# Kernel optimization log

Measured on AMD Instinct MI355X. Metric: run time of the kernel, lower is better.

The kernel has to match this reference:

```python
import jax, jax.numpy as jnp
import numpy as np

IN_DIM, OUT_DIM = 96, 32
D = IN_DIM + OUT_DIM  # 128, feature dim of x
H, KQ = 8, 64         # head_num, KQ_dim
GAMMA = 1e-4


def setup_inputs() -> dict:
    key = jax.random.key(0)
    kx, kk, kq, kv = jax.random.split(key, 4)
    B, N = 32, 2048
    std_kq = (GAMMA / D) ** 0.5
    return {
        "x": jax.random.normal(kx, (B, N, D), dtype=jnp.float32),
        # nn.Linear weight shape [out_features, in_features]; stacked per head
        "Wk": jax.random.normal(kk, (H, KQ, D), dtype=jnp.float32) * std_kq,
        "Wq": jax.random.normal(kq, (H, KQ, D), dtype=jnp.float32) * std_kq,
        "Wv": jax.random.normal(kv, (H, D, D), dtype=jnp.float32) * GAMMA,
    }


def reference(x, Wk, Wq, Wv):
    # Per-head projections (nn.Linear: y = x @ W^T), stacked over heads h
    K = jnp.einsum("bnd,hkd->bhnk", x, Wk)  # [B,H,N,KQ]
    Q = jnp.einsum("bnd,hkd->bhnk", x, Wq)  # [B,H,N,KQ]
    V = jnp.einsum("bnd,hed->bhne", x, Wv)  # [B,H,N,D]
    # No softmax -> (Q K^T) V == Q (K^T V); use the O(n d^2) associative form
    KtV = jnp.einsum("bhnk,bhne->bhke", K, V)  # [B,H,KQ,D]
    # sum over heads folded into the contraction
    out = jnp.einsum("bhnk,bhke->bne", Q, KtV)  # [B,N,D]
    return out
```

## Files before the change

### kernel.cpp

```cpp
#include <hip/hip_runtime.h>

#define BB 32
#define NN 2048
#define DD 128
#define HH 8
#define KK 64

typedef __attribute__((ext_vector_type(8))) short bf16x8;
typedef __attribute__((ext_vector_type(4))) float f32x4;
#define MFMA_BF16 __builtin_amdgcn_mfma_f32_16x16x32_bf16


__device__ __forceinline__ float bf2f(unsigned short h){ return __uint_as_float(((unsigned)h) << 16); }
__device__ __forceinline__ unsigned short f2bf(float f){
  unsigned u = __float_as_uint(f);
  u += 0x7fffu + ((u >> 16) & 1u);
  return (unsigned short)(u >> 16);
}
__device__ __forceinline__ unsigned pack2(float a, float b){
  return (unsigned)f2bf(a) | ((unsigned)f2bf(b) << 16);
}

__device__ __forceinline__ bf16x8 ldfrag_sw(const unsigned short* base, int row16, int kc, int lane){
  int d = row16 + (lane & 15);
  int q = lane >> 4;
  int ch = ((kc << 2) + q) ^ (d & 7);
  return *(const bf16x8*)(base + d*128 + ch*8);
}

__global__ __launch_bounds__(512, 4) void kgkp(const float* __restrict__ x,
                                               const float* __restrict__ Wq,
                                               const float* __restrict__ Wk,
                                               unsigned short* __restrict__ Gp_bf,
                                               unsigned short* __restrict__ Pbf,
                                               unsigned short* __restrict__ x_bf){
  __shared__ __align__(16) unsigned short sm[32768];
  const int t = threadIdx.x;
  const int bid = blockIdx.x;
  const int w = t >> 6, lane = t & 63, quad = lane >> 4;
  if (bid < 256){
    unsigned short* xh = sm;
    unsigned short* xl = sm + 16384;
    const int b = bid & 31, chunk = bid >> 5;
    const int wr = (w >> 1)*32, wc = (w & 1)*64;
    f32x4 acc[2][4] = {};
    for (int sub = 0; sub < 2; ++sub){
      if (sub) __syncthreads();
      const float* xb = x + ((size_t)b*NN + (size_t)(chunk*256 + sub*128))*DD;
      unsigned short* xbo = x_bf + (((size_t)(b*16 + chunk*2 + sub)) << 14);
      for (int it = 0; it < 2; ++it){
        int gidx = it*512 + t;
        int n4g = (gidx & 7) | (((gidx >> 6) & 3) << 3);
        int dcq = ((gidx >> 3) & 7) | (((gidx >> 8) & 3) << 3);
        float4 v[4];
        #pragma unroll
        for (int j = 0; j < 4; ++j)
          v[j] = *(const float4*)(xb + (size_t)(n4g*4 + j)*DD + dcq*4);
        unsigned short hh[4][4], ll[4][4];
        #pragma unroll
        for (int j = 0; j < 4; ++j)
          #pragma unroll
          for (int i = 0; i < 4; ++i){
            float f = (&v[j].x)[i];
            unsigned short h = f2bf(f);
            hh[j][i] = h;
            ll[j][i] = f2bf(f - bf2f(h));
          }
        #pragma unroll
        for (int i = 0; i < 4; ++i){
          int d = dcq*4 + i;
          int off = d*128 + ((((n4g >> 1) ^ (d & 7)) << 3) + (n4g & 1)*4);
          *(ushort4*)(xh + off) = make_ushort4(hh[0][i], hh[1][i], hh[2][i], hh[3][i]);
          *(ushort4*)(xl + off) = make_ushort4(ll[0][i], ll[1][i], ll[2][i], ll[3][i]);
        }
        #pragma unroll
        for (int j = 0; j < 4; ++j){
          int n = n4g*4 + j;
          int off = n*128 + ((((dcq >> 1) ^ (n & 7)) << 3) + (dcq & 1)*4);
          *(ushort4*)(xbo + off) = make_ushort4(hh[j][0], hh[j][1], hh[j][2], hh[j][3]);
        }
      }
      __syncthreads();
      for (int kc = 0; kc < 4; ++kc){
        bf16x8 ah[2], al[2], bh[4], bl[4];
        #pragma unroll
        for (int r = 0; r < 2; ++r){
          ah[r] = ldfrag_sw(xh, wr + r*16, kc, lane);
          al[r] = ldfrag_sw(xl, wr + r*16, kc, lane);
        }
        #pragma unroll
        for (int c = 0; c < 4; ++c){
          bh[c] = ldfrag_sw(xh, wc + c*16, kc, lane);
          bl[c] = ldfrag_sw(xl, wc + c*16, kc, lane);
        }
        #pragma unroll
        for (int r = 0; r < 2; ++r)
          #pragma unroll
          for (int c = 0; c < 4; ++c){
            acc[r][c] = MFMA_BF16(ah[r], bh[c], acc[r][c], 0, 0, 0);
            acc[r][c] = MFMA_BF16(ah[r], bl[c], acc[r][c], 0, 0, 0);
            acc[r][c] = MFMA_BF16(al[r], bh[c], acc[r][c], 0, 0, 0);
          }
      }
    }
    __syncthreads();
    float* Sf = (float*)sm;
    #pragma unroll
    for (int r = 0; r < 2; ++r)
      #pragma unroll
      for (int c = 0; c < 4; ++c)
        #pragma unroll
        for (int reg = 0; reg < 4; ++reg)
          Sf[(wr + r*16 + quad*4 + reg)*128 + wc + c*16 + (lane & 15)] = acc[r][c][reg];
    __syncthreads();
    unsigned short* gp = Gp_bf + ((size_t)(chunk*32 + b) << 14);
    for (int i = t; i < 2048; i += 512){
      int r = i >> 4, c8 = (i & 15) * 8;
      const float* s = Sf + r*128 + c8;
      uint4 o;
      o.x = pack2(s[0], s[1]); o.y = pack2(s[2], s[3]);
      o.z = pack2(s[4], s[5]); o.w = pack2(s[6], s[7]);
      *(uint4*)(gp + r*128 + c8) = o;
    }
  } else {
    float* Aq = (float*)sm;
    float* Bk = Aq + 64*36;
    const int kpid = bid - 256;
    const int h = kpid >> 2, rt = kpid & 3;
    const int i0 = rt * 32;
    const int tr = t >> 6, tc = t & 63;
    const float* wq = Wq + h*KK*DD;
    const float* wk = Wk + h*KK*DD;
    for (int i = t; i < 512; i += 512){
      int k = i >> 3, c4 = (i & 7) << 2;
      *(float4*)(&Aq[k*36 + c4]) = *(const float4*)(wq + k*DD + i0 + c4);
    }
    for (int i = t; i < 2048; i += 512){
      int k = i >> 5, c4 = (i & 31) << 2;
      *(float4*)(&Bk[k*132 + c4]) = *(const float4*)(wk + k*DD + c4);
    }
    __syncthreads();
    float acc[4][2] = {};
    for (int k = 0; k < 64; k += 2){
      float a0[4], a1[4], b0[2], b1[2];
      *(float4*)a0 = *(float4*)(&Aq[k*36 + tr*4]);
      *(float4*)a1 = *(float4*)(&Aq[(k+1)*36 + tr*4]);
      b0[0] = Bk[k*132 + tc*2];     b0[1] = Bk[k*132 + tc*2 + 1];
      b1[0] = Bk[(k+1)*132 + tc*2]; b1[1] = Bk[(k+1)*132 + tc*2 + 1];
      #pragma unroll
      for (int i = 0; i < 4; ++i)
        #pragma unroll
        for (int j = 0; j < 2; ++j){
          acc[i][j] += a0[i]*b0[j];
          acc[i][j] += a1[i]*b1[j];
        }
    }
    unsigned short* Ph = Pbf + h*DD*DD;
    #pragma unroll
    for (int i = 0; i < 4; ++i){
      int r = i0 + tr*4 + i, c = tc*2;
      int off = r*128 + ((((c >> 3) ^ (r & 7)) << 3) + (c & 7));
      *(ushort2*)(&Ph[off]) = make_ushort2(f2bf(acc[i][0]), f2bf(acc[i][1]));
    }
  }
}

__global__ __launch_bounds__(256) void kgr(const unsigned short* __restrict__ Gp_bf,
                                           const float* __restrict__ Wv,
                                           unsigned short* __restrict__ G_bf,
                                           unsigned short* __restrict__ Wv_bf){
  const int bid = blockIdx.x, t = threadIdx.x;
  if (bid < 256){
    const int b = bid >> 3, strip = bid & 7;
    const int r = strip*16 + (t >> 4), ch = t & 15;
    float s[8] = {};
    #pragma unroll
    for (int p = 0; p < 8; ++p){
      uint4 u = *(const uint4*)(Gp_bf + (((size_t)(p*32 + b)) << 14) + r*128 + ch*8);
      const unsigned short* pu = (const unsigned short*)&u;
      #pragma unroll
      for (int j = 0; j < 8; ++j) s[j] += bf2f(pu[j]);
    }
    uint4 o;
    o.x = pack2(s[0], s[1]); o.y = pack2(s[2], s[3]);
    o.z = pack2(s[4], s[5]); o.w = pack2(s[6], s[7]);
    *(uint4*)(G_bf + ((size_t)b << 14) + r*128 + ((ch ^ (r & 7)) << 3)) = o;
  } else {
    const int h = bid - 256;
    const float* Wvh = Wv + (size_t)h*DD*DD;
    unsigned short* outp = Wv_bf + (size_t)h*DD*DD;
    for (int i = t; i < 4096; i += 256){
      int e = i >> 5, dc = (i & 31) * 4;
      float4 v = *(const float4*)(Wvh + (size_t)e*DD + dc);
      int off = e*128 + ((((dc >> 3) ^ (e & 7)) << 3) + (dc & 4));
      *(ushort4*)(outp + off) = make_ushort4(f2bf(v.x), f2bf(v.y), f2bf(v.z), f2bf(v.w));
    }
  }
}

__global__ __launch_bounds__(512, 2) void km2(const unsigned short* __restrict__ G_bf,
                                              const unsigned short* __restrict__ Wv_bf,
                                              const unsigned short* __restrict__ Pbf,
                                              unsigned short* __restrict__ Mp_bf){
  __shared__ __align__(16) unsigned short sm[32768];
  unsigned short* As = sm;
  unsigned short* Bs = sm + 16384;
  const int bid = blockIdx.x;
  const int b = bid & 31, h = bid >> 5;
  const int t = threadIdx.x;
  const int w = t >> 6, lane = t & 63, quad = lane >> 4;
  const unsigned short* Gb = G_bf + ((size_t)b << 14);
  const unsigned short* Wvh = Wv_bf + ((size_t)h << 14);
  for (int i = t; i < 2048; i += 512){
    *(uint4*)(As + i*8) = *(const uint4*)(Gb + i*8);
    *(uint4*)(Bs + i*8) = *(const uint4*)(Wvh + i*8);
  }
  __syncthreads();
  f32x4 acc1[8] = {};
  for (int kc = 0; kc < 4; ++kc){
    bf16x8 a = ldfrag_sw(As, w*16, kc, lane);
    bf16x8 bb[8];
    #pragma unroll
    for (int c = 0; c < 8; ++c) bb[c] = ldfrag_sw(Bs, c*16, kc, lane);
    #pragma unroll
    for (int c = 0; c < 8; ++c) acc1[c] = MFMA_BF16(a, bb[c], acc1[c], 0, 0, 0);
  }
  __syncthreads();
  #pragma unroll
  for (int c = 0; c < 8; ++c){
    int e = c*16 + (lane & 15);
    int d0 = w*16 + quad*4;
    int off = e*128 + ((((d0 >> 3) ^ (e & 7)) << 3) + (d0 & 7));
    *(ushort4*)(Bs + off) = make_ushort4(f2bf(acc1[c][0]), f2bf(acc1[c][1]),
                                         f2bf(acc1[c][2]), f2bf(acc1[c][3]));
  }
  const unsigned short* Ph = Pbf + (size_t)h*DD*DD;
  for (int i = t; i < 2048; i += 512)
    *(uint4*)(As + i*8) = *(const uint4*)(Ph + i*8);
  __syncthreads();
  f32x4 acc2[8] = {};
  for (int kc = 0; kc < 4; ++kc){
    bf16x8 a = ldfrag_sw(As, w*16, kc, lane);
    bf16x8 bb[8];
    #pragma unroll
    for (int c = 0; c < 8; ++c) bb[c] = ldfrag_sw(Bs, c*16, kc, lane);
    #pragma unroll
    for (int c = 0; c < 8; ++c) acc2[c] = MFMA_BF16(a, bb[c], acc2[c], 0, 0, 0);
  }
  __syncthreads();
  float* Sf = (float*)sm;
  #pragma unroll
  for (int c = 0; c < 8; ++c)
    #pragma unroll
    for (int reg = 0; reg < 4; ++reg)
      Sf[(w*16 + quad*4 + reg)*128 + c*16 + (lane & 15)] = acc2[c][reg];
  __syncthreads();
  unsigned short* Mb = Mp_bf + (((size_t)(b*8 + h)) << 14);
  for (int i = t; i < 2048; i += 512){
    int r = i >> 4, c8 = (i & 15) * 8;
    const float* s = Sf + r*128 + c8;
    uint4 o;
    o.x = pack2(s[0], s[1]); o.y = pack2(s[2], s[3]);
    o.z = pack2(s[4], s[5]); o.w = pack2(s[6], s[7]);
    *(uint4*)(Mb + r*128 + c8) = o;
  }
}

__global__ __launch_bounds__(256) void kmr(const unsigned short* __restrict__ Mp_bf,
                                           unsigned short* __restrict__ Mt_sw){
  __shared__ float Sf[16][132];
  const int bid = blockIdx.x;
  const int b = bid >> 3, es = bid & 7;
  const int t = threadIdx.x;
  {
    int d = t >> 1, half = t & 1;
    float s[8] = {};
    #pragma unroll
    for (int h = 0; h < 8; ++h){
      uint4 u = *(const uint4*)(Mp_bf + (((size_t)(b*8 + h)) << 14) + d*128 + es*16 + half*8);
      const unsigned short* pu = (const unsigned short*)&u;
      #pragma unroll
      for (int j = 0; j < 8; ++j) s[j] += bf2f(pu[j]);
    }
    #pragma unroll
    for (int j = 0; j < 8; ++j) Sf[half*8 + j][d] = s[j];
  }
  __syncthreads();
  unsigned short* Mb = Mt_sw + ((size_t)b << 14);
  {
    int el = t >> 4, ng = t & 15;
    int e = es*16 + el;
    const float* s = &Sf[el][ng*8];
    uint4 o;
    o.x = pack2(s[0], s[1]); o.y = pack2(s[2], s[3]);
    o.z = pack2(s[4], s[5]); o.w = pack2(s[6], s[7]);
    *(uint4*)(Mb + e*128 + ((ng ^ (e & 7)) << 3)) = o;
  }
}

__global__ __launch_bounds__(512, 4) void ko2(const unsigned short* __restrict__ x_bf,
                                              const unsigned short* __restrict__ Mt_sw,
                                              float* __restrict__ out){
  __shared__ __align__(16) unsigned short sm[32768];
  unsigned short* xs = sm;
  unsigned short* Ms = sm + 16384;
  const int bid = blockIdx.x;
  const int b = bid & 31, nt = bid >> 5;
  const int t = threadIdx.x;
  const int w = t >> 6, lane = t & 63, quad = lane >> 4;
  const unsigned short* xbf = x_bf + (((size_t)(b*16 + nt)) << 14);
  const unsigned short* Mtb = Mt_sw + ((size_t)b << 14);
  for (int i = t; i < 2048; i += 512){
    *(uint4*)(xs + i*8) = *(const uint4*)(xbf + i*8);
    *(uint4*)(Ms + i*8) = *(const uint4*)(Mtb + i*8);
  }
  __syncthreads();
  const int wr = (w >> 1)*32, wc = (w & 1)*64;
  f32x4 acc[2][4] = {};
  for (int kc = 0; kc < 4; ++kc){
    bf16x8 a[2], bb[4];
    #pragma unroll
    for (int r = 0; r < 2; ++r) a[r] = ldfrag_sw(xs, wr + r*16, kc, lane);
    #pragma unroll
    for (int c = 0; c < 4; ++c) bb[c] = ldfrag_sw(Ms, wc + c*16, kc, lane);
    #pragma unroll
    for (int r = 0; r < 2; ++r)
      #pragma unroll
      for (int c = 0; c < 4; ++c)
        acc[r][c] = MFMA_BF16(a[r], bb[c], acc[r][c], 0, 0, 0);
  }
  __syncthreads();
  float* Sf = (float*)sm;
  #pragma unroll
  for (int r = 0; r < 2; ++r)
    #pragma unroll
    for (int c = 0; c < 4; ++c)
      #pragma unroll
      for (int reg = 0; reg < 4; ++reg)
        Sf[(wr + r*16 + quad*4 + reg)*128 + wc + c*16 + (lane & 15)] = acc[r][c][reg];
  __syncthreads();
  float* ob = out + ((size_t)b*NN + (size_t)nt*128)*DD;
  for (int i = t; i < 4096; i += 512){
    int n = i >> 5, c4 = (i & 31) * 4;
    *(float4*)(ob + (size_t)n*DD + c4) = *(const float4*)(Sf + n*128 + c4);
  }
}

extern "C" void kernel_launch(void* const* d_in, const int* in_sizes, int n_in,
                              void* d_out, int out_size, void* d_ws, size_t ws_size,
                              hipStream_t stream){
  const float* x  = (const float*)d_in[0];
  const float* Wk = (const float*)d_in[1];
  const float* Wq = (const float*)d_in[2];
  const float* Wv = (const float*)d_in[3];
  float* out = (float*)d_out;
  unsigned short* wsu = (unsigned short*)d_ws;
  unsigned short* Gp_bf = wsu;
  unsigned short* G_bf  = wsu + 4194304;
  unsigned short* Pbf   = wsu + 4718592;
  unsigned short* Wv_bf = wsu + 4849664;
  unsigned short* Mp_bf = wsu + 4980736;
  unsigned short* Mt_sw = wsu + 9175040;
  unsigned short* x_bf  = wsu + 9699328;

  kgkp<<<288, 512, 0, stream>>>(x, Wq, Wk, Gp_bf, Pbf, x_bf);
  kgr <<<264, 256, 0, stream>>>(Gp_bf, Wv, G_bf, Wv_bf);
  km2 <<<256, 512, 0, stream>>>(G_bf, Wv_bf, Pbf, Mp_bf);
  kmr <<<256, 256, 0, stream>>>(Mp_bf, Mt_sw);
  ko2 <<<512, 512, 0, stream>>>(x_bf, Mt_sw, out);
}
```

Baseline: 126.2 us.

## Fuse five kernel launches into one cooperative kernel with grid syncs

Merges the five pipeline kernels (Gram partials, reduction, M computation, head reduction, output GEMM) into a single cooperative kernel of 256 blocks separated by grid.sync barriers. The G reduction and the Wv bf16 conversion now happen directly into shared memory inside the M stage, which drops the G_bf/Wv_bf global round trips. The P computation is folded into the first 32 blocks, and the output stage processes two tiles per block. This removes launch gaps and some global traffic, but the final GEMM now has fewer resident blocks, grid barriers add cost, and the first 32 blocks carry extra serial work.

```diff
diff --git a/kernel.cpp b/kernel.cpp
--- a/kernel.cpp
+++ b/kernel.cpp
@@ -1,9 +1,10 @@
 #include <hip/hip_runtime.h>
-
-#define BB 32
+#include <hip/hip_cooperative_groups.h>
+
+namespace cg = cooperative_groups;
+
 #define NN 2048
 #define DD 128
-#define HH 8
 #define KK 64
 
 typedef __attribute__((ext_vector_type(8))) short bf16x8;
@@ -28,17 +29,21 @@
   return *(const bf16x8*)(base + d*128 + ch*8);
 }
 
-__global__ __launch_bounds__(512, 4) void kgkp(const float* __restrict__ x,
-                                               const float* __restrict__ Wq,
-                                               const float* __restrict__ Wk,
-                                               unsigned short* __restrict__ Gp_bf,
-                                               unsigned short* __restrict__ Pbf,
-                                               unsigned short* __restrict__ x_bf){
+__global__ __launch_bounds__(512, 2) void fused_all(
+    const float* __restrict__ x,  const float* __restrict__ Wq,
+    const float* __restrict__ Wk, const float* __restrict__ Wv,
+    float* __restrict__ out,
+    unsigned short* __restrict__ Gp_bf, unsigned short* __restrict__ Pbf,
+    unsigned short* __restrict__ Mp_bf, unsigned short* __restrict__ Mt_sw,
+    unsigned short* __restrict__ x_bf)
+{
   __shared__ __align__(16) unsigned short sm[32768];
   const int t = threadIdx.x;
   const int bid = blockIdx.x;
   const int w = t >> 6, lane = t & 63, quad = lane >> 4;
-  if (bid < 256){
+  cg::grid_group grid = cg::this_grid();
+
+  {
     unsigned short* xh = sm;
     unsigned short* xl = sm + 16384;
     const int b = bid & 31, chunk = bid >> 5;
@@ -122,227 +127,204 @@
       o.z = pack2(s[4], s[5]); o.w = pack2(s[6], s[7]);
       *(uint4*)(gp + r*128 + c8) = o;
     }
-  } else {
-    float* Aq = (float*)sm;
-    float* Bk = Aq + 64*36;
-    const int kpid = bid - 256;
-    const int h = kpid >> 2, rt = kpid & 3;
-    const int i0 = rt * 32;
-    const int tr = t >> 6, tc = t & 63;
-    const float* wq = Wq + h*KK*DD;
-    const float* wk = Wk + h*KK*DD;
-    for (int i = t; i < 512; i += 512){
-      int k = i >> 3, c4 = (i & 7) << 2;
-      *(float4*)(&Aq[k*36 + c4]) = *(const float4*)(wq + k*DD + i0 + c4);
-    }
+    if (bid < 32){
+      __syncthreads();
+      float* Aq = (float*)sm;
+      float* Bk = Aq + 64*36;
+      const int h = bid >> 2, rt = bid & 3;
+      const int i0 = rt * 32;
+      const int tr = t >> 6, tc = t & 63;
+      const float* wq = Wq + h*KK*DD;
+      const float* wk = Wk + h*KK*DD;
+      for (int i = t; i < 512; i += 512){
+        int k = i >> 3, c4 = (i & 7) << 2;
+        *(float4*)(&Aq[k*36 + c4]) = *(const float4*)(wq + k*DD + i0 + c4);
+      }
+      for (int i = t; i < 2048; i += 512){
+        int k = i >> 5, c4 = (i & 31) << 2;
+        *(float4*)(&Bk[k*132 + c4]) = *(const float4*)(wk + k*DD + c4);
+      }
+      __syncthreads();
+      float acc2[4][2] = {};
+      for (int k = 0; k < 64; k += 2){
+        float a0[4], a1[4], b0[2], b1[2];
+        *(float4*)a0 = *(float4*)(&Aq[k*36 + tr*4]);
+        *(float4*)a1 = *(float4*)(&Aq[(k+1)*36 + tr*4]);
+        b0[0] = Bk[k*132 + tc*2];     b0[1] = Bk[k*132 + tc*2 + 1];
+        b1[0] = Bk[(k+1)*132 + tc*2]; b1[1] = Bk[(k+1)*132 + tc*2 + 1];
+        #pragma unroll
+        for (int i = 0; i < 4; ++i)
+          #pragma unroll
+          for (int j = 0; j < 2; ++j){
+            acc2[i][j] += a0[i]*b0[j];
+            acc2[i][j] += a1[i]*b1[j];
+          }
+      }
+      unsigned short* Ph = Pbf + h*DD*DD;
+      #pragma unroll
+      for (int i = 0; i < 4; ++i){
+        int r = i0 + tr*4 + i, c = tc*2;
+        int off = r*128 + ((((c >> 3) ^ (r & 7)) << 3) + (c & 7));
+        *(ushort2*)(&Ph[off]) = make_ushort2(f2bf(acc2[i][0]), f2bf(acc2[i][1]));
+      }
+    }
+  }
+  __threadfence();
+  grid.sync();
+
+  {
+    unsigned short* As = sm;
+    unsigned short* Bs = sm + 16384;
+    const int b = bid & 31, h = bid >> 5;
     for (int i = t; i < 2048; i += 512){
-      int k = i >> 5, c4 = (i & 31) << 2;
-      *(float4*)(&Bk[k*132 + c4]) = *(const float4*)(wk + k*DD + c4);
-    }
-    __syncthreads();
-    float acc[4][2] = {};
-    for (int k = 0; k < 64; k += 2){
-      float a0[4], a1[4], b0[2], b1[2];
-      *(float4*)a0 = *(float4*)(&Aq[k*36 + tr*4]);
-      *(float4*)a1 = *(float4*)(&Aq[(k+1)*36 + tr*4]);
-      b0[0] = Bk[k*132 + tc*2];     b0[1] = Bk[k*132 + tc*2 + 1];
-      b1[0] = Bk[(k+1)*132 + tc*2]; b1[1] = Bk[(k+1)*132 + tc*2 + 1];
-      #pragma unroll
-      for (int i = 0; i < 4; ++i)
-        #pragma unroll
-        for (int j = 0; j < 2; ++j){
-          acc[i][j] += a0[i]*b0[j];
-          acc[i][j] += a1[i]*b1[j];
-        }
-    }
-    unsigned short* Ph = Pbf + h*DD*DD;
-    #pragma unroll
-    for (int i = 0; i < 4; ++i){
-      int r = i0 + tr*4 + i, c = tc*2;
-      int off = r*128 + ((((c >> 3) ^ (r & 7)) << 3) + (c & 7));
-      *(ushort2*)(&Ph[off]) = make_ushort2(f2bf(acc[i][0]), f2bf(acc[i][1]));
-    }
-  }
-}
-
-__global__ __launch_bounds__(256) void kgr(const unsigned short* __restrict__ Gp_bf,
-                                           const float* __restrict__ Wv,
-                                           unsigned short* __restrict__ G_bf,
-                                           unsigned short* __restrict__ Wv_bf){
-  const int bid = blockIdx.x, t = threadIdx.x;
-  if (bid < 256){
-    const int b = bid >> 3, strip = bid & 7;
-    const int r = strip*16 + (t >> 4), ch = t & 15;
-    float s[8] = {};
-    #pragma unroll
-    for (int p = 0; p < 8; ++p){
-      uint4 u = *(const uint4*)(Gp_bf + (((size_t)(p*32 + b)) << 14) + r*128 + ch*8);
-      const unsigned short* pu = (const unsigned short*)&u;
-      #pragma unroll
-      for (int j = 0; j < 8; ++j) s[j] += bf2f(pu[j]);
-    }
-    uint4 o;
-    o.x = pack2(s[0], s[1]); o.y = pack2(s[2], s[3]);
-    o.z = pack2(s[4], s[5]); o.w = pack2(s[6], s[7]);
-    *(uint4*)(G_bf + ((size_t)b << 14) + r*128 + ((ch ^ (r & 7)) << 3)) = o;
-  } else {
-    const int h = bid - 256;
+      int r = i >> 4, c8 = (i & 15) * 8;
+      float s[8] = {};
+      #pragma unroll
+      for (int p = 0; p < 8; ++p){
+        uint4 u = *(const uint4*)(Gp_bf + (((size_t)(p*32 + b)) << 14) + r*128 + c8);
+        const unsigned short* pu = (const unsigned short*)&u;
+        #pragma unroll
+        for (int j = 0; j < 8; ++j) s[j] += bf2f(pu[j]);
+      }
+      uint4 o;
+      o.x = pack2(s[0], s[1]); o.y = pack2(s[2], s[3]);
+      o.z = pack2(s[4], s[5]); o.w = pack2(s[6], s[7]);
+      *(uint4*)(As + r*128 + ((((c8 >> 3) ^ (r & 7))) << 3)) = o;
+    }
     const float* Wvh = Wv + (size_t)h*DD*DD;
-    unsigned short* outp = Wv_bf + (size_t)h*DD*DD;
-    for (int i = t; i < 4096; i += 256){
+    for (int i = t; i < 4096; i += 512){
       int e = i >> 5, dc = (i & 31) * 4;
       float4 v = *(const float4*)(Wvh + (size_t)e*DD + dc);
       int off = e*128 + ((((dc >> 3) ^ (e & 7)) << 3) + (dc & 4));
-      *(ushort4*)(outp + off) = make_ushort4(f2bf(v.x), f2bf(v.y), f2bf(v.z), f2bf(v.w));
+      *(ushort4*)(Bs + off) = make_ushort4(f2bf(v.x), f2bf(v.y), f2bf(v.z), f2bf(v.w));
+    }
+    __syncthreads();
+    f32x4 acc1[8] = {};
+    for (int kc = 0; kc < 4; ++kc){
+      bf16x8 a = ldfrag_sw(As, w*16, kc, lane);
+      bf16x8 bb[8];
+      #pragma unroll
+      for (int c = 0; c < 8; ++c) bb[c] = ldfrag_sw(Bs, c*16, kc, lane);
+      #pragma unroll
+      for (int c = 0; c < 8; ++c) acc1[c] = MFMA_BF16(a, bb[c], acc1[c], 0, 0, 0);
+    }
+    __syncthreads();
+    #pragma unroll
+    for (int c = 0; c < 8; ++c){
+      int e = c*16 + (lane & 15);
+      int d0 = w*16 + quad*4;
+      int off = e*128 + ((((d0 >> 3) ^ (e & 7)) << 3) + (d0 & 7));
+      *(ushort4*)(Bs + off) = make_ushort4(f2bf(acc1[c][0]), f2bf(acc1[c][1]),
+                                           f2bf(acc1[c][2]), f2bf(acc1[c][3]));
+    }
+    const unsigned short* Ph = Pbf + (size_t)h*DD*DD;
+    for (int i = t; i < 2048; i += 512)
+      *(uint4*)(As + i*8) = *(const uint4*)(Ph + i*8);
+    __syncthreads();
+    f32x4 acc2[8] = {};
+    for (int kc = 0; kc < 4; ++kc){
+      bf16x8 a = ldfrag_sw(As, w*16, kc, lane);
+      bf16x8 bb[8];
+      #pragma unroll
+      for (int c = 0; c < 8; ++c) bb[c] = ldfrag_sw(Bs, c*16, kc, lane);
+      #pragma unroll
+      for (int c = 0; c < 8; ++c) acc2[c] = MFMA_BF16(a, bb[c], acc2[c], 0, 0, 0);
+    }
+    __syncthreads();
+    float* Sf = (float*)sm;
+    #pragma unroll
+    for (int c = 0; c < 8; ++c)
+      #pragma unroll
+      for (int reg = 0; reg < 4; ++reg)
+        Sf[(w*16 + quad*4 + reg)*128 + c*16 + (lane & 15)] = acc2[c][reg];
+    __syncthreads();
+    unsigned short* Mb = Mp_bf + (((size_t)(b*8 + h)) << 14);
+    for (int i = t; i < 2048; i += 512){
+      int r = i >> 4, c8 = (i & 15) * 8;
+      const float* s = Sf + r*128 + c8;
+      uint4 o;
+      o.x = pack2(s[0], s[1]); o.y = pack2(s[2], s[3]);
+      o.z = pack2(s[4], s[5]); o.w = pack2(s[6], s[7]);
+      *(uint4*)(Mb + r*128 + c8) = o;
     }
   }
-}
-
-__global__ __launch_bounds__(512, 2) void km2(const unsigned short* __restrict__ G_bf,
-                                              const unsigned short* __restrict__ Wv_bf,
-                                              const unsigned short* __restrict__ Pbf,
-                                              unsigned short* __restrict__ Mp_bf){
-  __shared__ __align__(16) unsigned short sm[32768];
-  unsigned short* As = sm;
-  unsigned short* Bs = sm + 16384;
-  const int bid = blockIdx.x;
-  const int b = bid & 31, h = bid >> 5;
-  const int t = threadIdx.x;
-  const int w = t >> 6, lane = t & 63, quad = lane >> 4;
-  const unsigned short* Gb = G_bf + ((size_t)b << 14);
-  const unsigned short* Wvh = Wv_bf + ((size_t)h << 14);
-  for (int i = t; i < 2048; i += 512){
-    *(uint4*)(As + i*8) = *(const uint4*)(Gb + i*8);
-    *(uint4*)(Bs + i*8) = *(const uint4*)(Wvh + i*8);
+  __threadfence();
+  grid.sync();
+
+  {
+    const int rb = bid >> 3, es = bid & 7;
+    float* Rf = (float*)sm;
+    {
+      int d = t >> 2, q = t & 3;
+      float s[4] = {};
+      #pragma unroll
+      for (int h = 0; h < 8; ++h){
+        uint2 u = *(const uint2*)(Mp_bf + (((size_t)(rb*8 + h)) << 14) + d*128 + es*16 + q*4);
+        const unsigned short* pu = (const unsigned short*)&u;
+        #pragma unroll
+        for (int j = 0; j < 4; ++j) s[j] += bf2f(pu[j]);
+      }
+      #pragma unroll
+      for (int j = 0; j < 4; ++j) Rf[(q*4 + j)*132 + d] = s[j];
+    }
+    __syncthreads();
+    unsigned short* Mb = Mt_sw + ((size_t)rb << 14);
+    if (t < 256){
+      int el = t >> 4, ng = t & 15;
+      int e = es*16 + el;
+      const float* s2 = &Rf[el*132 + ng*8];
+      uint4 o;
+      o.x = pack2(s2[0], s2[1]); o.y = pack2(s2[2], s2[3]);
+      o.z = pack2(s2[4], s2[5]); o.w = pack2(s2[6], s2[7]);
+      *(uint4*)(Mb + e*128 + ((ng ^ (e & 7)) << 3)) = o;
+    }
   }
-  __syncthreads();
-  f32x4 acc1[8] = {};
-  for (int kc = 0; kc < 4; ++kc){
-    bf16x8 a = ldfrag_sw(As, w*16, kc, lane);
-    bf16x8 bb[8];
-    #pragma unroll
-    for (int c = 0; c < 8; ++c) bb[c] = ldfrag_sw(Bs, c*16, kc, lane);
-    #pragma unroll
-    for (int c = 0; c < 8; ++c) acc1[c] = MFMA_BF16(a, bb[c], acc1[c], 0, 0, 0);
-  }
-  __syncthreads();
-  #pragma unroll
-  for (int c = 0; c < 8; ++c){
-    int e = c*16 + (lane & 15);
-    int d0 = w*16 + quad*4;
-    int off = e*128 + ((((d0 >> 3) ^ (e & 7)) << 3) + (d0 & 7));
-    *(ushort4*)(Bs + off) = make_ushort4(f2bf(acc1[c][0]), f2bf(acc1[c][1]),
-                                         f2bf(acc1[c][2]), f2bf(acc1[c][3]));
-  }
-  const unsigned short* Ph = Pbf + (size_t)h*DD*DD;
-  for (int i = t; i < 2048; i += 512)
-    *(uint4*)(As + i*8) = *(const uint4*)(Ph + i*8);
-  __syncthreads();
-  f32x4 acc2[8] = {};
-  for (int kc = 0; kc < 4; ++kc){
-    bf16x8 a = ldfrag_sw(As, w*16, kc, lane);
-    bf16x8 bb[8];
-    #pragma unroll
-    for (int c = 0; c < 8; ++c) bb[c] = ldfrag_sw(Bs, c*16, kc, lane);
-    #pragma unroll
-    for (int c = 0; c < 8; ++c) acc2[c] = MFMA_BF16(a, bb[c], acc2[c], 0, 0, 0);
-  }
-  __syncthreads();
-  float* Sf = (float*)sm;
-  #pragma unroll
-  for (int c = 0; c < 8; ++c)
-    #pragma unroll
-    for (int reg = 0; reg < 4; ++reg)
-      Sf[(w*16 + quad*4 + reg)*128 + c*16 + (lane & 15)] = acc2[c][reg];
-  __syncthreads();
-  unsigned short* Mb = Mp_bf + (((size_t)(b*8 + h)) << 14);
-  for (int i = t; i < 2048; i += 512){
-    int r = i >> 4, c8 = (i & 15) * 8;
-    const float* s = Sf + r*128 + c8;
-    uint4 o;
-    o.x = pack2(s[0], s[1]); o.y = pack2(s[2], s[3]);
-    o.z = pack2(s[4], s[5]); o.w = pack2(s[6], s[7]);
-    *(uint4*)(Mb + r*128 + c8) = o;
-  }
-}
-
-__global__ __launch_bounds__(256) void kmr(const unsigned short* __restrict__ Mp_bf,
-                                           unsigned short* __restrict__ Mt_sw){
-  __shared__ float Sf[16][132];
-  const int bid = blockIdx.x;
-  const int b = bid >> 3, es = bid & 7;
-  const int t = threadIdx.x;
+  __threadfence();
+  grid.sync();
+
   {
-    int d = t >> 1, half = t & 1;
-    float s[8] = {};
-    #pragma unroll
-    for (int h = 0; h < 8; ++h){
-      uint4 u = *(const uint4*)(Mp_bf + (((size_t)(b*8 + h)) << 14) + d*128 + es*16 + half*8);
-      const unsigned short* pu = (const unsigned short*)&u;
-      #pragma unroll
-      for (int j = 0; j < 8; ++j) s[j] += bf2f(pu[j]);
-    }
-    #pragma unroll
-    for (int j = 0; j < 8; ++j) Sf[half*8 + j][d] = s[j];
-  }
-  __syncthreads();
-  unsigned short* Mb = Mt_sw + ((size_t)b << 14);
-  {
-    int el = t >> 4, ng = t & 15;
-    int e = es*16 + el;
-    const float* s = &Sf[el][ng*8];
-    uint4 o;
-    o.x = pack2(s[0], s[1]); o.y = pack2(s[2], s[3]);
-    o.z = pack2(s[4], s[5]); o.w = pack2(s[6], s[7]);
-    *(uint4*)(Mb + e*128 + ((ng ^ (e & 7)) << 3)) = o;
-  }
-}
-
-__global__ __launch_bounds__(512, 4) void ko2(const unsigned short* __restrict__ x_bf,
-                                              const unsigned short* __restrict__ Mt_sw,
-                                              float* __restrict__ out){
-  __shared__ __align__(16) unsigned short sm[32768];
-  unsigned short* xs = sm;
-  unsigned short* Ms = sm + 16384;
-  const int bid = blockIdx.x;
-  const int b = bid & 31, nt = bid >> 5;
-  const int t = threadIdx.x;
-  const int w = t >> 6, lane = t & 63, quad = lane >> 4;
-  const unsigned short* xbf = x_bf + (((size_t)(b*16 + nt)) << 14);
-  const unsigned short* Mtb = Mt_sw + ((size_t)b << 14);
-  for (int i = t; i < 2048; i += 512){
-    *(uint4*)(xs + i*8) = *(const uint4*)(xbf + i*8);
-    *(uint4*)(Ms + i*8) = *(const uint4*)(Mtb + i*8);
-  }
-  __syncthreads();
-  const int wr = (w >> 1)*32, wc = (w & 1)*64;
-  f32x4 acc[2][4] = {};
-  for (int kc = 0; kc < 4; ++kc){
-    bf16x8 a[2], bb[4];
-    #pragma unroll
-    for (int r = 0; r < 2; ++r) a[r] = ldfrag_sw(xs, wr + r*16, kc, lane);
-    #pragma unroll
-    for (int c = 0; c < 4; ++c) bb[c] = ldfrag_sw(Ms, wc + c*16, kc, lane);
-    #pragma unroll
-    for (int r = 0; r < 2; ++r)
-      #pragma unroll
-      for (int c = 0; c < 4; ++c)
-        acc[r][c] = MFMA_BF16(a[r], bb[c], acc[r][c], 0, 0, 0);
-  }
-  __syncthreads();
-  float* Sf = (float*)sm;
-  #pragma unroll
-  for (int r = 0; r < 2; ++r)
-    #pragma unroll
-    for (int c = 0; c < 4; ++c)
-      #pragma unroll
-      for (int reg = 0; reg < 4; ++reg)
-        Sf[(wr + r*16 + quad*4 + reg)*128 + wc + c*16 + (lane & 15)] = acc[r][c][reg];
-  __syncthreads();
-  float* ob = out + ((size_t)b*NN + (size_t)nt*128)*DD;
-  for (int i = t; i < 4096; i += 512){
-    int n = i >> 5, c4 = (i & 31) * 4;
-    *(float4*)(ob + (size_t)n*DD + c4) = *(const float4*)(Sf + n*128 + c4);
+    const int b = bid & 31, ntb = (bid >> 5) * 2;
+    const unsigned short* Mtb = Mt_sw + ((size_t)b << 14);
+    for (int nt = ntb; nt < ntb + 2; ++nt){
+      __syncthreads();
+      unsigned short* xs = sm;
+      unsigned short* Ms = sm + 16384;
+      const unsigned short* xbf = x_bf + (((size_t)(b*16 + nt)) << 14);
+      for (int i = t; i < 2048; i += 512){
+        *(uint4*)(xs + i*8) = *(const uint4*)(xbf + i*8);
+        *(uint4*)(Ms + i*8) = *(const uint4*)(Mtb + i*8);
+      }
+      __syncthreads();
+      const int wr = (w >> 1)*32, wc = (w & 1)*64;
+      f32x4 acc[2][4] = {};
+      for (int kc = 0; kc < 4; ++kc){
+        bf16x8 a[2], bb[4];
+        #pragma unroll
+        for (int r = 0; r < 2; ++r) a[r] = ldfrag_sw(xs, wr + r*16, kc, lane);
+        #pragma unroll
+        for (int c = 0; c < 4; ++c) bb[c] = ldfrag_sw(Ms, wc + c*16, kc, lane);
+        #pragma unroll
+        for (int r = 0; r < 2; ++r)
+          #pragma unroll
+          for (int c = 0; c < 4; ++c)
+            acc[r][c] = MFMA_BF16(a[r], bb[c], acc[r][c], 0, 0, 0);
+      }
+      __syncthreads();
+      float* Sf = (float*)sm;
+      #pragma unroll
+      for (int r = 0; r < 2; ++r)
+        #pragma unroll
+        for (int c = 0; c < 4; ++c)
+          #pragma unroll
+          for (int reg = 0; reg < 4; ++reg)
+            Sf[(wr + r*16 + quad*4 + reg)*128 + wc + c*16 + (lane & 15)] = acc[r][c][reg];
+      __syncthreads();
+      float* ob = out + ((size_t)b*NN + (size_t)nt*128)*DD;
+      for (int i = t; i < 4096; i += 512){
+        int n = i >> 5, c4 = (i & 31) * 4;
+        *(float4*)(ob + (size_t)n*DD + c4) = *(const float4*)(Sf + n*128 + c4);
+      }
+    }
   }
 }
 
@@ -356,16 +338,12 @@
   float* out = (float*)d_out;
   unsigned short* wsu = (unsigned short*)d_ws;
   unsigned short* Gp_bf = wsu;
-  unsigned short* G_bf  = wsu + 4194304;
-  unsigned short* Pbf   = wsu + 4718592;
-  unsigned short* Wv_bf = wsu + 4849664;
-  unsigned short* Mp_bf = wsu + 4980736;
-  unsigned short* Mt_sw = wsu + 9175040;
-  unsigned short* x_bf  = wsu + 9699328;
-
-  kgkp<<<288, 512, 0, stream>>>(x, Wq, Wk, Gp_bf, Pbf, x_bf);
-  kgr <<<264, 256, 0, stream>>>(Gp_bf, Wv, G_bf, Wv_bf);
-  km2 <<<256, 512, 0, stream>>>(G_bf, Wv_bf, Pbf, Mp_bf);
-  kmr <<<256, 256, 0, stream>>>(Mp_bf, Mt_sw);
-  ko2 <<<512, 512, 0, stream>>>(x_bf, Mt_sw, out);
-}
+  unsigned short* Pbf   = wsu + 4194304;
+  unsigned short* Mp_bf = wsu + 4325376;
+  unsigned short* Mt_sw = wsu + 8519680;
+  unsigned short* x_bf  = wsu + 9043968;
+
+  void* args[] = { (void*)&x, (void*)&Wq, (void*)&Wk, (void*)&Wv, (void*)&out,
+                   (void*)&Gp_bf, (void*)&Pbf, (void*)&Mp_bf, (void*)&Mt_sw, (void*)&x_bf };
+  hipLaunchCooperativeKernel((const void*)fused_all, dim3(256), dim3(512), args, 0, stream);
+}
```

Result: slower. 359.9 us (+185.2%).

## Fuse Gram reduction and Wv conversion into km2, split Gram over more blocks

Applied to the files above, without the earlier changes.

The Gram-matrix kernel now launches 512 blocks of 128 rows each instead of 256 blocks of 256 rows, which gives more parallelism. The separate reduce/convert kernel is removed: km2 now sums the 16 partial Gram matrices and converts its Wv slice to bf16 straight into shared memory. km2 is also split over two output-column halves to reach 512 blocks with higher occupancy. The cost is redundant work: each km2 block re-reads all 16 partials, so the reduction traffic is duplicated across heads and halves, and Wv is converted repeatedly.

```diff
diff --git a/kernel.cpp b/kernel.cpp
--- a/kernel.cpp
+++ b/kernel.cpp
@@ -1,9 +1,7 @@
 #include <hip/hip_runtime.h>
 
-#define BB 32
 #define NN 2048
 #define DD 128
-#define HH 8
 #define KK 64
 
 typedef __attribute__((ext_vector_type(8))) short bf16x8;
@@ -38,70 +36,67 @@
   const int t = threadIdx.x;
   const int bid = blockIdx.x;
   const int w = t >> 6, lane = t & 63, quad = lane >> 4;
-  if (bid < 256){
+  if (bid < 512){
     unsigned short* xh = sm;
     unsigned short* xl = sm + 16384;
     const int b = bid & 31, chunk = bid >> 5;
     const int wr = (w >> 1)*32, wc = (w & 1)*64;
     f32x4 acc[2][4] = {};
-    for (int sub = 0; sub < 2; ++sub){
-      if (sub) __syncthreads();
-      const float* xb = x + ((size_t)b*NN + (size_t)(chunk*256 + sub*128))*DD;
-      unsigned short* xbo = x_bf + (((size_t)(b*16 + chunk*2 + sub)) << 14);
-      for (int it = 0; it < 2; ++it){
-        int gidx = it*512 + t;
-        int n4g = (gidx & 7) | (((gidx >> 6) & 3) << 3);
-        int dcq = ((gidx >> 3) & 7) | (((gidx >> 8) & 3) << 3);
-        float4 v[4];
-        #pragma unroll
-        for (int j = 0; j < 4; ++j)
-          v[j] = *(const float4*)(xb + (size_t)(n4g*4 + j)*DD + dcq*4);
-        unsigned short hh[4][4], ll[4][4];
-        #pragma unroll
-        for (int j = 0; j < 4; ++j)
-          #pragma unroll
-          for (int i = 0; i < 4; ++i){
-            float f = (&v[j].x)[i];
-            unsigned short h = f2bf(f);
-            hh[j][i] = h;
-            ll[j][i] = f2bf(f - bf2f(h));
-          }
+    const float* xb = x + ((size_t)b*NN + (size_t)chunk*128)*DD;
+    unsigned short* xbo = x_bf + (((size_t)(b*16 + chunk)) << 14);
+    for (int it = 0; it < 2; ++it){
+      int gidx = it*512 + t;
+      int n4g = (gidx & 7) | (((gidx >> 6) & 3) << 3);
+      int dcq = ((gidx >> 3) & 7) | (((gidx >> 8) & 3) << 3);
+      float4 v[4];
+      #pragma unroll
+      for (int j = 0; j < 4; ++j)
+        v[j] = *(const float4*)(xb + (size_t)(n4g*4 + j)*DD + dcq*4);
+      unsigned short hh[4][4], ll[4][4];
+      #pragma unroll
+      for (int j = 0; j < 4; ++j)
         #pragma unroll
         for (int i = 0; i < 4; ++i){
-          int d = dcq*4 + i;
-          int off = d*128 + ((((n4g >> 1) ^ (d & 7)) << 3) + (n4g & 1)*4);
-          *(ushort4*)(xh + off) = make_ushort4(hh[0][i], hh[1][i], hh[2][i], hh[3][i]);
-          *(ushort4*)(xl + off) = make_ushort4(ll[0][i], ll[1][i], ll[2][i], ll[3][i]);
+          float f = (&v[j].x)[i];
+          unsigned short h = f2bf(f);
+          hh[j][i] = h;
+          ll[j][i] = f2bf(f - bf2f(h));
         }
-        #pragma unroll
-        for (int j = 0; j < 4; ++j){
-          int n = n4g*4 + j;
-          int off = n*128 + ((((dcq >> 1) ^ (n & 7)) << 3) + (dcq & 1)*4);
-          *(ushort4*)(xbo + off) = make_ushort4(hh[j][0], hh[j][1], hh[j][2], hh[j][3]);
-        }
+      #pragma unroll
+      for (int i = 0; i < 4; ++i){
+        int d = dcq*4 + i;
+        int off = d*128 + ((((n4g >> 1) ^ (d & 7)) << 3) + (n4g & 1)*4);
+        *(ushort4*)(xh + off) = make_ushort4(hh[0][i], hh[1][i], hh[2][i], hh[3][i]);
+        *(ushort4*)(xl + off) = make_ushort4(ll[0][i], ll[1][i], ll[2][i], ll[3][i]);
       }
-      __syncthreads();
-      for (int kc = 0; kc < 4; ++kc){
-        bf16x8 ah[2], al[2], bh[4], bl[4];
-        #pragma unroll
-        for (int r = 0; r < 2; ++r){
-          ah[r] = ldfrag_sw(xh, wr + r*16, kc, lane);
-          al[r] = ldfrag_sw(xl, wr + r*16, kc, lane);
-        }
+      #pragma unroll
+      for (int j = 0; j < 4; ++j){
+        int n = n4g*4 + j;
+        int off = n*128 + ((((dcq >> 1) ^ (n & 7)) << 3) + (dcq & 1)*4);
+        *(ushort4*)(xbo + off) = make_ushort4(hh[j][0], hh[j][1], hh[j][2], hh[j][3]);
+      }
+    }
+    __syncthreads();
+    for (int kc = 0; kc < 4; ++kc){
+      bf16x8 ah[2], al[2], bh[4], bl[4];
+      #pragma unroll
+      for (int r = 0; r < 2; ++r){
+        ah[r] = ldfrag_sw(xh, wr + r*16, kc, lane);
+        al[r] = ldfrag_sw(xl, wr + r*16, kc, lane);
+      }
+      #pragma unroll
+      for (int c = 0; c < 4; ++c){
+        bh[c] = ldfrag_sw(xh, wc + c*16, kc, lane);
+        bl[c] = ldfrag_sw(xl, wc + c*16, kc, lane);
+      }
+      #pragma unroll
+      for (int r = 0; r < 2; ++r)
         #pragma unroll
         for (int c = 0; c < 4; ++c){
-          bh[c] = ldfrag_sw(xh, wc + c*16, kc, lane);
-          bl[c] = ldfrag_sw(xl, wc + c*16, kc, lane);
+          acc[r][c] = MFMA_BF16(ah[r], bh[c], acc[r][c], 0, 0, 0);
+          acc[r][c] = MFMA_BF16(ah[r], bl[c], acc[r][c], 0, 0, 0);
+          acc[r][c] = MFMA_BF16(al[r], bh[c], acc[r][c], 0, 0, 0);
         }
-        #pragma unroll
-        for (int r = 0; r < 2; ++r)
-          #pragma unroll
-          for (int c = 0; c < 4; ++c){
-            acc[r][c] = MFMA_BF16(ah[r], bh[c], acc[r][c], 0, 0, 0);
-            acc[r][c] = MFMA_BF16(ah[r], bl[c], acc[r][c], 0, 0, 0);
-            acc[r][c] = MFMA_BF16(al[r], bh[c], acc[r][c], 0, 0, 0);
-          }
-      }
     }
     __syncthreads();
     float* Sf = (float*)sm;
@@ -125,7 +120,7 @@
   } else {
     float* Aq = (float*)sm;
     float* Bk = Aq + 64*36;
-    const int kpid = bid - 256;
+    const int kpid = bid - 512;
     const int h = kpid >> 2, rt = kpid & 3;
     const int i0 = rt * 32;
     const int tr = t >> 6, tc = t & 63;
@@ -165,18 +160,23 @@
   }
 }
 
-__global__ __launch_bounds__(256) void kgr(const unsigned short* __restrict__ Gp_bf,
-                                           const float* __restrict__ Wv,
-                                           unsigned short* __restrict__ G_bf,
-                                           unsigned short* __restrict__ Wv_bf){
-  const int bid = blockIdx.x, t = threadIdx.x;
-  if (bid < 256){
-    const int b = bid >> 3, strip = bid & 7;
-    const int r = strip*16 + (t >> 4), ch = t & 15;
+__global__ __launch_bounds__(512, 4) void km2(const unsigned short* __restrict__ Gp_bf,
+                                              const float* __restrict__ Wv,
+                                              const unsigned short* __restrict__ Pbf,
+                                              unsigned short* __restrict__ Mp_bf){
+  __shared__ __align__(16) unsigned short sm[24576];
+  unsigned short* As = sm;
+  unsigned short* Bs = sm + 16384;
+  const int bid = blockIdx.x;
+  const int b = bid & 31, h = (bid >> 5) & 7, eh = bid >> 8;
+  const int t = threadIdx.x;
+  const int w = t >> 6, lane = t & 63, quad = lane >> 4;
+  for (int i = t; i < 2048; i += 512){
+    int r = i >> 4, c8 = (i & 15) * 8;
     float s[8] = {};
     #pragma unroll
-    for (int p = 0; p < 8; ++p){
-      uint4 u = *(const uint4*)(Gp_bf + (((size_t)(p*32 + b)) << 14) + r*128 + ch*8);
+    for (int p = 0; p < 16; ++p){
+      uint4 u = *(const uint4*)(Gp_bf + (((size_t)(p*32 + b)) << 14) + r*128 + c8);
       const unsigned short* pu = (const unsigned short*)&u;
       #pragma unroll
       for (int j = 0; j < 8; ++j) s[j] += bf2f(pu[j]);
@@ -184,50 +184,28 @@
     uint4 o;
     o.x = pack2(s[0], s[1]); o.y = pack2(s[2], s[3]);
     o.z = pack2(s[4], s[5]); o.w = pack2(s[6], s[7]);
-    *(uint4*)(G_bf + ((size_t)b << 14) + r*128 + ((ch ^ (r & 7)) << 3)) = o;
-  } else {
-    const int h = bid - 256;
-    const float* Wvh = Wv + (size_t)h*DD*DD;
-    unsigned short* outp = Wv_bf + (size_t)h*DD*DD;
-    for (int i = t; i < 4096; i += 256){
-      int e = i >> 5, dc = (i & 31) * 4;
-      float4 v = *(const float4*)(Wvh + (size_t)e*DD + dc);
-      int off = e*128 + ((((dc >> 3) ^ (e & 7)) << 3) + (dc & 4));
-      *(ushort4*)(outp + off) = make_ushort4(f2bf(v.x), f2bf(v.y), f2bf(v.z), f2bf(v.w));
-    }
-  }
-}
-
-__global__ __launch_bounds__(512, 2) void km2(const unsigned short* __restrict__ G_bf,
-                                              const unsigned short* __restrict__ Wv_bf,
-                                              const unsigned short* __restrict__ Pbf,
-                                              unsigned short* __restrict__ Mp_bf){
-  __shared__ __align__(16) unsigned short sm[32768];
-  unsigned short* As = sm;
-  unsigned short* Bs = sm + 16384;
-  const int bid = blockIdx.x;
-  const int b = bid & 31, h = bid >> 5;
-  const int t = threadIdx.x;
-  const int w = t >> 6, lane = t & 63, quad = lane >> 4;
-  const unsigned short* Gb = G_bf + ((size_t)b << 14);
-  const unsigned short* Wvh = Wv_bf + ((size_t)h << 14);
+    *(uint4*)(As + r*128 + ((((c8 >> 3) ^ (r & 7))) << 3)) = o;
+  }
+  const float* Wvh = Wv + (size_t)h*DD*DD + (size_t)eh*64*DD;
   for (int i = t; i < 2048; i += 512){
-    *(uint4*)(As + i*8) = *(const uint4*)(Gb + i*8);
-    *(uint4*)(Bs + i*8) = *(const uint4*)(Wvh + i*8);
-  }
-  __syncthreads();
-  f32x4 acc1[8] = {};
+    int el = i >> 5, dc = (i & 31) * 4;
+    float4 v = *(const float4*)(Wvh + (size_t)el*DD + dc);
+    int off = el*128 + ((((dc >> 3) ^ (el & 7)) << 3) + (dc & 4));
+    *(ushort4*)(Bs + off) = make_ushort4(f2bf(v.x), f2bf(v.y), f2bf(v.z), f2bf(v.w));
+  }
+  __syncthreads();
+  f32x4 acc1[4] = {};
   for (int kc = 0; kc < 4; ++kc){
     bf16x8 a = ldfrag_sw(As, w*16, kc, lane);
-    bf16x8 bb[8];
-    #pragma unroll
-    for (int c = 0; c < 8; ++c) bb[c] = ldfrag_sw(Bs, c*16, kc, lane);
-    #pragma unroll
-    for (int c = 0; c < 8; ++c) acc1[c] = MFMA_BF16(a, bb[c], acc1[c], 0, 0, 0);
+    bf16x8 bb[4];
+    #pragma unroll
+    for (int c = 0; c < 4; ++c) bb[c] = ldfrag_sw(Bs, c*16, kc, lane);
+    #pragma unroll
+    for (int c = 0; c < 4; ++c) acc1[c] = MFMA_BF16(a, bb[c], acc1[c], 0, 0, 0);
   }
   __syncthreads();
   #pragma unroll
-  for (int c = 0; c < 8; ++c){
+  for (int c = 0; c < 4; ++c){
     int e = c*16 + (lane & 15);
     int d0 = w*16 + quad*4;
     int off = e*128 + ((((d0 >> 3) ^ (e & 7)) << 3) + (d0 & 7));
@@ -238,27 +216,27 @@
   for (int i = t; i < 2048; i += 512)
     *(uint4*)(As + i*8) = *(const uint4*)(Ph + i*8);
   __syncthreads();
-  f32x4 acc2[8] = {};
+  f32x4 acc2[4] = {};
   for (int kc = 0; kc < 4; ++kc){
     bf16x8 a = ldfrag_sw(As, w*16, kc, lane);
-    bf16x8 bb[8];
-    #pragma unroll
-    for (int c = 0; c < 8; ++c) bb[c] = ldfrag_sw(Bs, c*16, kc, lane);
-    #pragma unroll
-    for (int c = 0; c < 8; ++c) acc2[c] = MFMA_BF16(a, bb[c], acc2[c], 0, 0, 0);
+    bf16x8 bb[4];
+    #pragma unroll
+    for (int c = 0; c < 4; ++c) bb[c] = ldfrag_sw(Bs, c*16, kc, lane);
+    #pragma unroll
+    for (int c = 0; c < 4; ++c) acc2[c] = MFMA_BF16(a, bb[c], acc2[c], 0, 0, 0);
   }
   __syncthreads();
   float* Sf = (float*)sm;
   #pragma unroll
-  for (int c = 0; c < 8; ++c)
+  for (int c = 0; c < 4; ++c)
     #pragma unroll
     for (int reg = 0; reg < 4; ++reg)
-      Sf[(w*16 + quad*4 + reg)*128 + c*16 + (lane & 15)] = acc2[c][reg];
-  __syncthreads();
-  unsigned short* Mb = Mp_bf + (((size_t)(b*8 + h)) << 14);
-  for (int i = t; i < 2048; i += 512){
-    int r = i >> 4, c8 = (i & 15) * 8;
-    const float* s = Sf + r*128 + c8;
+      Sf[(w*16 + quad*4 + reg)*64 + c*16 + (lane & 15)] = acc2[c][reg];
+  __syncthreads();
+  unsigned short* Mb = Mp_bf + (((size_t)(b*8 + h)) << 14) + eh*64;
+  for (int i = t; i < 1024; i += 512){
+    int r = i >> 3, c8 = (i & 7) * 8;
+    const float* s = Sf + r*64 + c8;
     uint4 o;
     o.x = pack2(s[0], s[1]); o.y = pack2(s[2], s[3]);
     o.z = pack2(s[4], s[5]); o.w = pack2(s[6], s[7]);
@@ -356,16 +334,13 @@
   float* out = (float*)d_out;
   unsigned short* wsu = (unsigned short*)d_ws;
   unsigned short* Gp_bf = wsu;
-  unsigned short* G_bf  = wsu + 4194304;
-  unsigned short* Pbf   = wsu + 4718592;
-  unsigned short* Wv_bf = wsu + 4849664;
-  unsigned short* Mp_bf = wsu + 4980736;
-  unsigned short* Mt_sw = wsu + 9175040;
-  unsigned short* x_bf  = wsu + 9699328;
-
-  kgkp<<<288, 512, 0, stream>>>(x, Wq, Wk, Gp_bf, Pbf, x_bf);
-  kgr <<<264, 256, 0, stream>>>(Gp_bf, Wv, G_bf, Wv_bf);
-  km2 <<<256, 512, 0, stream>>>(G_bf, Wv_bf, Pbf, Mp_bf);
+  unsigned short* Pbf   = wsu + 8388608;
+  unsigned short* Mp_bf = wsu + 8519680;
+  unsigned short* Mt_sw = wsu + 12713984;
+  unsigned short* x_bf  = wsu + 13238272;
+
+  kgkp<<<544, 512, 0, stream>>>(x, Wq, Wk, Gp_bf, Pbf, x_bf);
+  km2 <<<512, 512, 0, stream>>>(Gp_bf, Wv, Pbf, Mp_bf);
   kmr <<<256, 256, 0, stream>>>(Mp_bf, Mt_sw);
   ko2 <<<512, 512, 0, stream>>>(x_bf, Mt_sw, out);
 }
```

After: 131.2 us. 1.04x slower.
